# Performance work log

Hardware: AMD Instinct MI355X
Metric: run time of the kernel (lower is better)

The kernel has to match this reference:

```python
import jax, jax.numpy as jnp
import numpy as np

POOL = 4
SCALE = 1.0 / 16.0
B, C, H, W = 64, 256, 36, 36
NC = POOL * POOL           # 16 correlation channels
RED = 4                    # SE reduction
INTER = NC // 2            # non-local inter channels = 8


def _hat_cumint(t):
    # integral of hat kernel max(0,1-|s|) over (-inf, t]
    t = jnp.clip(t, -1.0, 1.0)
    return jnp.where(t < 0.0, 0.5 * (t + 1.0) ** 2, 1.0 - 0.5 * (1.0 - t) ** 2)


def _axis_weights(lo, hi, n):
    # lo, hi: (B, P) bin edges in feature coords -> (B, P, n) exact integral
    # of the bilinear (hat) basis of each integer sample i over [lo, hi].
    i = jnp.arange(n, dtype=lo.dtype)
    return _hat_cumint(hi[..., None] - i) - _hat_cumint(lo[..., None] - i)


def prroi_pool(feat, rois_xyxy, pool, scale):
    # Precise RoI Pooling: analytic integral of bilinear interpolation per bin.
    Bn, Cn, Hn, Wn = feat.shape
    x1 = rois_xyxy[:, 0] * scale
    y1 = rois_xyxy[:, 1] * scale
    x2 = rois_xyxy[:, 2] * scale
    y2 = rois_xyxy[:, 3] * scale
    bw = (x2 - x1) / pool
    bh = (y2 - y1) / pool
    k = jnp.arange(pool, dtype=feat.dtype)
    ax = x1[:, None] + k * bw[:, None]
    bx = ax + bw[:, None]
    ay = y1[:, None] + k * bh[:, None]
    by = ay + bh[:, None]
    Wx = _axis_weights(ax, bx, Wn)   # (B, P, W)
    Wy = _axis_weights(ay, by, Hn)   # (B, P, H)
    pooled = jnp.einsum('bchw,bph,bqw->bcpq', feat, Wy, Wx)
    area = (bw * bh)[:, None, None, None]
    return jnp.where(area > 0, pooled / jnp.maximum(area, 1e-12), 0.0)


def setup_inputs() -> dict:
    key = jax.random.key(0)
    ks = jax.random.split(key, 12)
    feat1 = jax.random.normal(ks[0], (B, C, H, W), jnp.float32)
    feat2 = jax.random.normal(ks[1], (B, C, H, W), jnp.float32)
    # valid (x, y, w, h) boxes inside a 576px image
    xy = jax.random.uniform(ks[2], (B, 2), jnp.float32, 0.0, 416.0)
    wh = jax.random.uniform(ks[3], (B, 2), jnp.float32, 32.0, 160.0)
    bb1 = jnp.concatenate([xy, wh], axis=1)[None]  # (1, B, 4)

    def conv_init(k, shape):  # normal(0, sqrt(2/(kh*kw*out)))
        n = shape[0]  # 1x1 convs: kh*kw*out_ch = out_ch
        return jax.random.normal(k, shape, jnp.float32) * np.sqrt(2.0 / n)

    se_w1 = conv_init(ks[4], (NC // RED, NC))
    se_w2 = conv_init(ks[5], (NC, NC // RED))
    nl_theta_w = conv_init(ks[6], (INTER, NC))
    nl_phi_w = conv_init(ks[7], (INTER, NC))
    nl_g_w = conv_init(ks[8], (INTER, NC))
    nl_W_w = conv_init(ks[9], (NC, INTER))
    zi = jnp.zeros((INTER,), jnp.float32)
    zc = jnp.zeros((NC,), jnp.float32)
    return {
        'feat1': feat1, 'feat2': feat2, 'bb1': bb1,
        'se_w1': se_w1, 'se_w2': se_w2,
        'nl_theta_w': nl_theta_w, 'nl_theta_b': zi,
        'nl_phi_w': nl_phi_w, 'nl_phi_b': zi,
        'nl_g_w': nl_g_w, 'nl_g_b': zi,
        'nl_W_w': nl_W_w, 'nl_W_b': zc,
    }


def reference(feat1, feat2, bb1, se_w1, se_w2, nl_theta_w, nl_theta_b,
              nl_phi_w, nl_phi_b, nl_g_w, nl_g_b, nl_W_w, nl_W_b):
    boxes = bb1[0]  # (B, 4) xywh
    xyxy = jnp.concatenate([boxes[:, :2], boxes[:, :2] + boxes[:, 2:4]], axis=1)
    ker = prroi_pool(feat1, xyxy, POOL, SCALE)          # (B, C, P, P)
    Bn, Cn, Hn, Wn = feat2.shape
    kflat = ker.reshape(Bn, Cn, NC)
    # pixel_corr: per-sample 1x1 conv == batched GEMM
    corr = jnp.einsum('bchw,bck->bkhw', feat2, kflat)   # (B, 16, H, W)
    # SE channel attention
    s = corr.mean(axis=(2, 3))                          # (B, 16)
    s = jax.nn.sigmoid(jax.nn.relu(s @ se_w1.T) @ se_w2.T)
    x = corr * s[:, :, None, None]
    # Non-local (embedded gaussian) spatial attention
    xf = x.reshape(Bn, NC, Hn * Wn)                     # (B, 16, N)
    theta = jnp.einsum('oc,bcn->bno', nl_theta_w, xf) + nl_theta_b     # (B, N, 8)
    phi = jnp.einsum('oc,bcn->bon', nl_phi_w, xf) + nl_phi_b[:, None]  # (B, 8, N)
    g = jnp.einsum('oc,bcn->bno', nl_g_w, xf) + nl_g_b                 # (B, N, 8)
    attn = jax.nn.softmax(jnp.einsum('bno,bom->bnm', theta, phi), axis=-1)
    y = jnp.einsum('bnm,bmo->bno', attn, g)             # (B, N, 8)
    z = jnp.einsum('co,bno->bcn', nl_W_w, y) + nl_W_b[:, None]
    return z.reshape(Bn, NC, Hn, Wn) + x
```

## Files before the change

### kernel.cpp

```cpp
#include <hip/hip_runtime.h>
#include <cmath>

#define NB 64
#define NCC 256
#define NH 36
#define NW 36
#define NHW 1296
#define NK 16
#define NI 8
#define SC (1.0f/16.0f)
#define LOG2E 1.4426950408889634f
#define NPAD 1312

typedef __attribute__((ext_vector_type(16))) float f32x16;
typedef __attribute__((ext_vector_type(4)))  float f32x4;
typedef __attribute__((ext_vector_type(4)))  short s16x4;
typedef __attribute__((ext_vector_type(8)))  unsigned short u16x8;
typedef __attribute__((ext_vector_type(2)))  unsigned int u32x2;

__device__ __forceinline__ float hatc(float t){
  t = fminf(fmaxf(t, -1.0f), 1.0f);
  float a = 1.0f + t, bq = 1.0f - t;
  return (t < 0.0f) ? 0.5f*a*a : 1.0f - 0.5f*bq*bq;
}

__device__ __forceinline__ unsigned short bf16rn(float f){
  unsigned int u = __builtin_bit_cast(unsigned int, f);
  return (unsigned short)((u + 0x7FFFu + ((u >> 16) & 1u)) >> 16);
}
__device__ __forceinline__ float bf16tof(unsigned short h){
  unsigned int u = ((unsigned int)h) << 16;
  return __builtin_bit_cast(float, u);
}

__global__ __launch_bounds__(256) void k_prpool(const float* __restrict__ feat1,
    const float* __restrict__ bb1, float* __restrict__ kflat){
  int blk = blockIdx.x;
  int b = blk >> 6, cg = blk & 63;
  int t = threadIdx.x, w = t >> 6, lane = t & 63;
  int c = cg*4 + w;
  __shared__ float4 wY4[36];
  __shared__ float  wXp[36*5];
  float bx = bb1[b*4+0], by = bb1[b*4+1], bwv = bb1[b*4+2], bhv = bb1[b*4+3];
  float x1 = bx*SC, y1 = by*SC;
  float binw = bwv*SC*0.25f, binh = bhv*SC*0.25f;
  if (t < 36){
    float fi = (float)t;
    float4 r;
    r.x = hatc(y1 + 1.0f*binh - fi) - hatc(y1 + 0.0f*binh - fi);
    r.y = hatc(y1 + 2.0f*binh - fi) - hatc(y1 + 1.0f*binh - fi);
    r.z = hatc(y1 + 3.0f*binh - fi) - hatc(y1 + 2.0f*binh - fi);
    r.w = hatc(y1 + 4.0f*binh - fi) - hatc(y1 + 3.0f*binh - fi);
    wY4[t] = r;
  } else if (t < 72){
    int i = t - 36;
    float fi = (float)i;
    wXp[i*5+0] = hatc(x1 + 1.0f*binw - fi) - hatc(x1 + 0.0f*binw - fi);
    wXp[i*5+1] = hatc(x1 + 2.0f*binw - fi) - hatc(x1 + 1.0f*binw - fi);
    wXp[i*5+2] = hatc(x1 + 3.0f*binw - fi) - hatc(x1 + 2.0f*binw - fi);
    wXp[i*5+3] = hatc(x1 + 4.0f*binw - fi) - hatc(x1 + 3.0f*binw - fi);
  }
  __syncthreads();
  f32x4 acc4[4];
  #pragma unroll
  for (int p=0;p<4;p++) acc4[p] = (f32x4){0,0,0,0};
  const float4* fp4 = (const float4*)(feat1 + ((size_t)(b*256+c))*NHW);

  auto body = [&](float4 v, int px){
    #pragma unroll
    for (int j=0;j<4;j++){
      int p = px + j;
      int h = p/36, x = p - h*36;
      float vj = (j==0)?v.x:(j==1)?v.y:(j==2)?v.z:v.w;
      float4 wy = wY4[h];
      f32x4 wxv = {wXp[x*5+0], wXp[x*5+1], wXp[x*5+2], wXp[x*5+3]};
      f32x4 a0 = {vj*wy.x, vj*wy.x, vj*wy.x, vj*wy.x};
      f32x4 a1 = {vj*wy.y, vj*wy.y, vj*wy.y, vj*wy.y};
      f32x4 a2 = {vj*wy.z, vj*wy.z, vj*wy.z, vj*wy.z};
      f32x4 a3 = {vj*wy.w, vj*wy.w, vj*wy.w, vj*wy.w};
      acc4[0] = __builtin_elementwise_fma(a0, wxv, acc4[0]);
      acc4[1] = __builtin_elementwise_fma(a1, wxv, acc4[1]);
      acc4[2] = __builtin_elementwise_fma(a2, wxv, acc4[2]);
      acc4[3] = __builtin_elementwise_fma(a3, wxv, acc4[3]);
    }
  };

  #pragma unroll
  for (int i=0;i<5;i++){
    int f4i = i*64 + lane;
    float4 v = fp4[f4i];
    body(v, f4i*4);
  }
  if (lane < 4){
    int f4i = 320 + lane;
    float4 v = fp4[f4i];
    body(v, f4i*4);
  }
  float accf[16];
  #pragma unroll
  for (int p=0;p<4;p++){
    accf[p*4+0]=acc4[p].x; accf[p*4+1]=acc4[p].y;
    accf[p*4+2]=acc4[p].z; accf[p*4+3]=acc4[p].w;
  }
  #pragma unroll
  for (int k=0;k<16;k++){
    float a = accf[k];
    #pragma unroll
    for (int off=32; off>0; off>>=1) a += __shfl_down(a, off);
    accf[k] = a;
  }
  if (lane == 0){
    float area = binw*binh;
    float ia = (area > 0.0f) ? 1.0f/fmaxf(area,1e-12f) : 0.0f;
    float4* kp = (float4*)(kflat + ((size_t)(b*256+c))*16);
    kp[0] = make_float4(accf[0]*ia, accf[1]*ia, accf[2]*ia, accf[3]*ia);
    kp[1] = make_float4(accf[4]*ia, accf[5]*ia, accf[6]*ia, accf[7]*ia);
    kp[2] = make_float4(accf[8]*ia, accf[9]*ia, accf[10]*ia, accf[11]*ia);
    kp[3] = make_float4(accf[12]*ia, accf[13]*ia, accf[14]*ia, accf[15]*ia);
  }
}

__global__ __launch_bounds__(512) void k_corr(const float* __restrict__ feat2,
    const float* __restrict__ kflat, float* __restrict__ corr,
    float* __restrict__ partial_se){
  int blk = blockIdx.x;
  int b = blk / 6, ch = blk - b*6;
  int t = threadIdx.x, w = t >> 6, lane = t & 63;
  int px0 = ch*216;
  __shared__ float par[4][16][216];

  int wu = __builtin_amdgcn_readfirstlane(w);
  int c0 = wu*32;
  int l4 = (lane < 54) ? lane : 53;

  f32x4 acc[16];
  #pragma unroll
  for (int k=0;k<16;k++) acc[k] = (f32x4){0,0,0,0};

  const float* f2base = feat2 + (size_t)b*NCC*NHW + px0 + l4*4;
  const float* kfb = kflat + (size_t)b*4096;
  #pragma unroll 4
  for (int c = c0; c < c0+32; ++c){
    f32x4 r = *(const f32x4*)(f2base + (size_t)c*NHW);
    f32x16 kf = *(const f32x16*)(kfb + c*16);
    #pragma unroll
    for (int k=0;k<16;k++){
      f32x4 kv = {kf[k], kf[k], kf[k], kf[k]};
      acc[k] = __builtin_elementwise_fma(r, kv, acc[k]);
    }
  }

  if (w >= 4){
    #pragma unroll
    for (int k=0;k<16;k++)
      *(f32x4*)&par[w-4][k][l4*4] = acc[k];
  }
  __syncthreads();
  if (w < 4){
    #pragma unroll
    for (int k=0;k<16;k++){
      f32x4 tmp = *(const f32x4*)&par[w][k][l4*4];
      *(f32x4*)&par[w][k][l4*4] = tmp + acc[k];
    }
  }
  __syncthreads();
  int k = (w<<1) | (lane>>5);
  int j0 = lane & 31;
  float se_r = 0.0f;
  float* cp = corr + (size_t)b*NK*NHW + (size_t)k*NHW + px0;
  for (int jj=j0; jj<54; jj+=32){
    f32x4 s = *(const f32x4*)&par[0][k][jj*4];
    s += *(const f32x4*)&par[1][k][jj*4];
    s += *(const f32x4*)&par[2][k][jj*4];
    s += *(const f32x4*)&par[3][k][jj*4];
    *(f32x4*)(cp + jj*4) = s;
    se_r += (s.x+s.y) + (s.z+s.w);
  }
  #pragma unroll
  for (int off=16; off>0; off>>=1) se_r += __shfl_down(se_r, off, 32);
  if (j0 == 0)
    partial_se[(size_t)blk*16 + k] = se_r;
}

__global__ __launch_bounds__(64) void k_tpg(const float* __restrict__ corr,
    const float* __restrict__ partial_se,
    const float* __restrict__ w1, const float* __restrict__ w2,
    const float* __restrict__ tw, const float* __restrict__ tb,
    const float* __restrict__ pw, const float* __restrict__ pb,
    const float* __restrict__ gw, const float* __restrict__ gb,
    float* __restrict__ sscale,
    unsigned short* __restrict__ thetaX, unsigned short* __restrict__ phiX,
    unsigned short* __restrict__ gT){
  int blk = blockIdx.x;
  int b = blk/21, ch = blk - b*21;
  int t = threadIdx.x;
  __shared__ float Wt[128], Wp[128], Wg[128], Bz[24], Ss[16], sS[16], sR[4];
  for (int i=t; i<128; i+=64){ Wt[i]=tw[i]; Wp[i]=pw[i]; Wg[i]=gw[i]; }
  if (t < 8){ Bz[t]=tb[t]; Bz[8+t]=pb[t]; Bz[16+t]=gb[t]; }
  if (t < 16){
    float a = 0.f;
    #pragma unroll
    for (int c2=0; c2<6; c2++) a += partial_se[(size_t)(b*6+c2)*16 + t];
    sS[t] = a * (1.0f/1296.0f);
  }
  __syncthreads();
  if (t < 4){
    float a=0.f;
    #pragma unroll
    for (int k=0;k<16;k++) a += sS[k]*w1[t*16+k];
    sR[t] = fmaxf(a, 0.f);
  }
  __syncthreads();
  if (t < 16){
    float a=0.f;
    #pragma unroll
    for (int j=0;j<4;j++) a += sR[j]*w2[t*4+j];
    float gsc = 1.0f/(1.0f+__expf(-a));
    Ss[t] = gsc;
    if (ch == 0) sscale[b*16+t] = gsc;
  }
  __syncthreads();
  int n = ch*64 + t;
  if (n >= NHW) return;
  float x[16];
  const float* cp = corr + (size_t)b*NK*NHW + n;
  #pragma unroll
  for (int c=0;c<16;c++) x[c] = cp[(size_t)c*NHW] * Ss[c];
  float th[8], ph[8], gg[8];
  #pragma unroll
  for (int o=0;o<8;o++){
    float a=Bz[o], p2=Bz[8+o], gq=Bz[16+o];
    #pragma unroll
    for (int c=0;c<16;c++){
      a  += Wt[o*16+c]*x[c];
      p2 += Wp[o*16+c]*x[c];
      gq += Wg[o*16+c]*x[c];
    }
    th[o]=a*LOG2E; ph[o]=p2; gg[o]=gq;
  }
  unsigned short tH[8], tL[8], pH[8], pL[8];
  #pragma unroll
  for (int o=0;o<8;o++){
    unsigned short hh = bf16rn(th[o]);
    tH[o] = hh; tL[o] = bf16rn(th[o] - bf16tof(hh));
    unsigned short ph2 = bf16rn(ph[o]);
    pH[o] = ph2; pL[o] = bf16rn(ph[o] - bf16tof(ph2));
  }
  {
    u16x8* tp = (u16x8*)(thetaX + ((size_t)b*NPAD + n)*16);
    tp[0] = (u16x8){tH[0],tH[1],tH[2],tH[3], tL[0],tL[1],tL[2],tL[3]};
    tp[1] = (u16x8){tH[4],tH[5],tH[6],tH[7], tL[4],tL[5],tL[6],tL[7]};
    u16x8* pp = (u16x8*)(phiX + ((size_t)b*NPAD + n)*16);
    pp[0] = (u16x8){pH[0],pH[1],pH[2],pH[3], pL[0],pL[1],pL[2],pL[3]};
    pp[1] = (u16x8){pH[4],pH[5],pH[6],pH[7], pL[4],pL[5],pL[6],pL[7]};
  }
  #pragma unroll
  for (int o=0;o<8;o++)
    gT[((size_t)b*16 + o)*NPAD + n] = bf16rn(gg[o]);
  gT[((size_t)b*16 + 8)*NPAD + n] = 0x3F80;
}

__global__ __launch_bounds__(128) void k_attn(
    const unsigned short* __restrict__ thetaX, const unsigned short* __restrict__ phiX,
    const unsigned short* __restrict__ gT,
    const float* __restrict__ corr, const float* __restrict__ sscale,
    const float* __restrict__ Ww, const float* __restrict__ Wb,
    float* __restrict__ out){
  int blk = blockIdx.x;
  int b = blk / 41, qb = blk - b*41;
  int t = threadIdx.x, w = t >> 6, lane = t & 63;
  int h = lane >> 5, r31 = lane & 31;
  __shared__ float smm[2][32];
  __shared__ float sY[16][64];
  __shared__ float yl[32][12];

  const unsigned short* thx = thetaX + (size_t)b*NPAD*16;
  const unsigned short* phx = phiX   + (size_t)b*NPAD*16;

  s16x4 Bh, Bl;
  {
    u16x8 tv = *(const u16x8*)(thx + ((size_t)(qb*32 + r31))*16 + h*8);
    Bh = (s16x4){(short)tv[0],(short)tv[1],(short)tv[2],(short)tv[3]};
    Bl = (s16x4){(short)tv[4],(short)tv[5],(short)tv[6],(short)tv[7]};
  }

  int kt0 = w ? 21 : 0;
  int ktN = w ? 41 : 21;

  float m = -1e30f;
  for (int kt = kt0; kt < ktN; ++kt){
    u16x8 av = *(const u16x8*)(phx + ((size_t)(kt*32 + r31))*16 + h*8);
    s16x4 Ah = (s16x4){(short)av[0],(short)av[1],(short)av[2],(short)av[3]};
    f32x16 S = __builtin_amdgcn_mfma_f32_32x32x8bf16_1k(Ah, Bh, (f32x16)(0.0f), 0, 0, 0);
    if (kt != 40){
      #pragma unroll
      for (int r=0;r<16;r++) m = fmaxf(m, S[r]);
    } else {
      #pragma unroll
      for (int r=0;r<8;r++) m = fmaxf(m, S[r]);
    }
  }
  m = fmaxf(m, __shfl_xor(m, 32));
  if (h == 0) smm[w][r31] = m;
  __syncthreads();
  m = fmaxf(smm[0][r31], smm[1][r31]);

  f32x16 Y = (f32x16)(0.0f);
  int colc = (r31 < 9) ? r31 : 0;
  const unsigned short* gb2 = gT + ((size_t)b*16 + colc)*NPAD;

  for (int kt = kt0; kt < ktN; ++kt){
    u16x8 av = *(const u16x8*)(phx + ((size_t)(kt*32 + r31))*16 + h*8);
    s16x4 Ah = (s16x4){(short)av[0],(short)av[1],(short)av[2],(short)av[3]};
    s16x4 Al = (s16x4){(short)av[4],(short)av[5],(short)av[6],(short)av[7]};
    f32x16 S = __builtin_amdgcn_mfma_f32_32x32x8bf16_1k(Ah, Bl, (f32x16)(0.0f), 0, 0, 0);
    S = __builtin_amdgcn_mfma_f32_32x32x8bf16_1k(Al, Bh, S, 0, 0, 0);
    S = __builtin_amdgcn_mfma_f32_32x32x8bf16_1k(Ah, Bh, S, 0, 0, 0);
    if (kt == 40){
      #pragma unroll
      for (int r=8;r<16;r++) S[r] = -1e30f;
    }
    float p[16];
    #pragma unroll
    for (int r=0;r<16;r++) p[r] = __builtin_amdgcn_exp2f(S[r] - m);
    unsigned int c[8];
    #pragma unroll
    for (int i=0;i<8;i++){
      unsigned int cc;
      asm("v_cvt_pk_bf16_f32 %0, %1, %2" : "=v"(cc) : "v"(p[2*i]), "v"(p[2*i+1]));
      c[i] = cc;
    }
    #pragma unroll
    for (int mf=0; mf<4; ++mf){
      s16x4 Ap = __builtin_bit_cast(s16x4, (u32x2){c[2*mf], c[2*mf+1]});
      u32x2 vv = *(const u32x2*)(gb2 + kt*32 + mf*8 + h*4);
      s16x4 Vb = __builtin_bit_cast(s16x4, vv);
      Y = __builtin_amdgcn_mfma_f32_32x32x8bf16_1k(Ap, Vb, Y, 0, 0, 0);
    }
  }

  if (w == 1){
    #pragma unroll
    for (int r=0;r<16;r++) sY[r][lane] = Y[r];
  }
  __syncthreads();
  if (w == 0){
    #pragma unroll
    for (int r=0;r<16;r++) Y[r] += sY[r][lane];
    if (r31 < 9){
      #pragma unroll
      for (int r=0;r<16;r++){
        int q = (r&3) + 8*(r>>2) + 4*h;
        yl[q][r31] = Y[r];
      }
    }
  }
  __syncthreads();

  int q = t & 31, cg = t >> 5;
  int n = qb*32 + q;
  if (n < NHW){
    float il = 1.0f / yl[q][8];
    float yv[8];
    #pragma unroll
    for (int o=0;o<8;o++) yv[o] = yl[q][o] * il;
    const float* cp = corr + (size_t)b*NK*NHW + n;
    const float* ss = sscale + b*16;
    float* op = out + (size_t)b*NK*NHW + n;
    #pragma unroll
    for (int i=0;i<4;i++){
      int c2 = cg*4 + i;
      float z = Wb[c2];
      #pragma unroll
      for (int o=0;o<8;o++) z += Ww[c2*8+o]*yv[o];
      op[(size_t)c2*NHW] = z + cp[(size_t)c2*NHW]*ss[c2];
    }
  }
}

extern "C" void kernel_launch(void* const* d_in, const int* in_sizes, int n_in,
                              void* d_out, int out_size, void* d_ws, size_t ws_size,
                              hipStream_t stream){
  const float* feat1 = (const float*)d_in[0];
  const float* feat2 = (const float*)d_in[1];
  const float* bb1   = (const float*)d_in[2];
  const float* se_w1 = (const float*)d_in[3];
  const float* se_w2 = (const float*)d_in[4];
  const float* tw    = (const float*)d_in[5];
  const float* tb    = (const float*)d_in[6];
  const float* pw    = (const float*)d_in[7];
  const float* pb    = (const float*)d_in[8];
  const float* gw    = (const float*)d_in[9];
  const float* gb    = (const float*)d_in[10];
  const float* Ww    = (const float*)d_in[11];
  const float* Wb    = (const float*)d_in[12];
  float* out = (float*)d_out;

  float* ws = (float*)d_ws;
  float* kflat      = ws;
  float* corr       = kflat + 64*256*16;
  float* partial_se = corr + (size_t)64*16*1296;
  float* sscale     = partial_se + 64*6*16;
  unsigned short* thetaX = (unsigned short*)(sscale + 64*16);
  unsigned short* phiX   = thetaX + (size_t)64*NPAD*16;
  unsigned short* gT     = phiX   + (size_t)64*NPAD*16;

  hipLaunchKernelGGL(k_prpool, dim3(64*64), dim3(256), 0, stream, feat1, bb1, kflat);
  hipLaunchKernelGGL(k_corr, dim3(64*6), dim3(512), 0, stream, feat2, kflat, corr, partial_se);
  hipLaunchKernelGGL(k_tpg, dim3(64*21), dim3(64), 0, stream, corr, partial_se,
                     se_w1, se_w2, tw, tb, pw, pb, gw, gb, sscale, thetaX, phiX, gT);
  hipLaunchKernelGGL(k_attn, dim3(64*41), dim3(128), 0, stream,
                     thetaX, phiX, gT, corr, sscale, Ww, Wb, out);
}
```

Before: 123.0 us.

## Split attention key range across two blocks with flash-style partial merge

The non-local attention kernel is split into a partial kernel that processes half of the key tiles per block, doubling the grid, and writes per-query row max and unnormalized Y partials to workspace. A second finalize kernel rescales and merges the two partials and then applies the output projection and residual. The aim is more parallelism and occupancy for the long per-block key loop, at the cost of an extra launch and workspace traffic.

New measurement: 108.3 us. -11.9%, faster.

```diff
diff --git a/kernel.cpp b/kernel.cpp
--- a/kernel.cpp
+++ b/kernel.cpp
@@ -260,14 +260,13 @@
   gT[((size_t)b*16 + 8)*NPAD + n] = 0x3F80;
 }
 
-__global__ __launch_bounds__(128) void k_attn(
+__global__ __launch_bounds__(128) void k_attn_part(
     const unsigned short* __restrict__ thetaX, const unsigned short* __restrict__ phiX,
     const unsigned short* __restrict__ gT,
-    const float* __restrict__ corr, const float* __restrict__ sscale,
-    const float* __restrict__ Ww, const float* __restrict__ Wb,
-    float* __restrict__ out){
+    float* __restrict__ mpart, float* __restrict__ Ypart){
   int blk = blockIdx.x;
-  int b = blk / 41, qb = blk - b*41;
+  int b = blk / 82, rem = blk - b*82;
+  int qb = rem >> 1, kh = rem & 1;
   int t = threadIdx.x, w = t >> 6, lane = t & 63;
   int h = lane >> 5, r31 = lane & 31;
   __shared__ float smm[2][32];
@@ -284,8 +283,11 @@
     Bl = (s16x4){(short)tv[4],(short)tv[5],(short)tv[6],(short)tv[7]};
   }
 
-  int kt0 = w ? 21 : 0;
-  int ktN = w ? 41 : 21;
+  int kbeg = kh ? 21 : 0;
+  int kend = kh ? 41 : 21;
+  int kmid = kh ? 31 : 11;
+  int kt0 = w ? kmid : kbeg;
+  int ktN = w ? kend : kmid;
 
   float m = -1e30f;
   for (int kt = kt0; kt < ktN; ++kt){
@@ -304,6 +306,8 @@
   if (h == 0) smm[w][r31] = m;
   __syncthreads();
   m = fmaxf(smm[0][r31], smm[1][r31]);
+  if (w == 0 && h == 0)
+    mpart[((size_t)((b*41 + qb)*2 + kh))*32 + r31] = m;
 
   f32x16 Y = (f32x16)(0.0f);
   int colc = (r31 < 9) ? r31 : 0;
@@ -354,6 +358,40 @@
         yl[q][r31] = Y[r];
       }
     }
+  }
+  __syncthreads();
+
+  float* yp = Ypart + (size_t)((b*41 + qb)*2 + kh)*288;
+  for (int i = t; i < 288; i += 128){
+    int q = i / 9, c2 = i - q*9;
+    yp[i] = yl[q][c2];
+  }
+}
+
+__global__ __launch_bounds__(128) void k_attn_fin(
+    const float* __restrict__ mpart, const float* __restrict__ Ypart,
+    const float* __restrict__ corr, const float* __restrict__ sscale,
+    const float* __restrict__ Ww, const float* __restrict__ Wb,
+    float* __restrict__ out){
+  int blk = blockIdx.x;
+  int b = blk / 41, qb = blk - b*41;
+  int t = threadIdx.x;
+  __shared__ float yl[32][9];
+  __shared__ float cf0[32], cf1[32];
+  size_t p2 = (size_t)(b*41 + qb)*2;
+  if (t < 32){
+    float m0 = mpart[p2*32 + t];
+    float m1 = mpart[(p2+1)*32 + t];
+    float M = fmaxf(m0, m1);
+    cf0[t] = __builtin_amdgcn_exp2f(m0 - M);
+    cf1[t] = __builtin_amdgcn_exp2f(m1 - M);
+  }
+  __syncthreads();
+  const float* y0 = Ypart + p2*288;
+  const float* y1 = Ypart + (p2+1)*288;
+  for (int i = t; i < 288; i += 128){
+    int q = i / 9;
+    ((float*)yl)[i] = y0[i]*cf0[q] + y1[i]*cf1[q];
   }
   __syncthreads();
 
@@ -404,11 +442,15 @@
   unsigned short* thetaX = (unsigned short*)(sscale + 64*16);
   unsigned short* phiX   = thetaX + (size_t)64*NPAD*16;
   unsigned short* gT     = phiX   + (size_t)64*NPAD*16;
+  float* mpart = (float*)(gT + (size_t)64*16*NPAD);
+  float* Ypart = mpart + (size_t)64*41*2*32;
 
   hipLaunchKernelGGL(k_prpool, dim3(64*64), dim3(256), 0, stream, feat1, bb1, kflat);
   hipLaunchKernelGGL(k_corr, dim3(64*6), dim3(512), 0, stream, feat2, kflat, corr, partial_se);
   hipLaunchKernelGGL(k_tpg, dim3(64*21), dim3(64), 0, stream, corr, partial_se,
                      se_w1, se_w2, tw, tb, pw, pb, gw, gb, sscale, thetaX, phiX, gT);
-  hipLaunchKernelGGL(k_attn, dim3(64*41), dim3(128), 0, stream,
-                     thetaX, phiX, gT, corr, sscale, Ww, Wb, out);
-}
+  hipLaunchKernelGGL(k_attn_part, dim3(64*82), dim3(128), 0, stream,
+                     thetaX, phiX, gT, mpart, Ypart);
+  hipLaunchKernelGGL(k_attn_fin, dim3(64*41), dim3(128), 0, stream,
+                     mpart, Ypart, corr, sscale, Ww, Wb, out);
+}
```
